# Performance work log

Hardware: AMD Instinct MI355X
Metric: run time of the kernel (lower is better)

Reference implementation:

```python
import jax, jax.numpy as jnp
import numpy as np

N, E, D_IN, D_H, D_OUT = 8000, 256000, 128, 128, 64
TEMP = 10.0       # config temperature.value (non-learnable)
WEIGHT = 1.0      # config weight.value (non-learnable)
LN_EPS = 1e-5


def _gcn_conv(x, W, b, src, dst, n):
    # PyG GCNConv: add self loops, sym-normalized aggregation, then bias.
    h = x @ W
    loop = jnp.arange(n)
    s = jnp.concatenate([src, loop])
    d = jnp.concatenate([dst, loop])
    deg = jnp.zeros((n,), h.dtype).at[d].add(1.0)
    dinv = jax.lax.rsqrt(jnp.maximum(deg, 1e-12))
    norm = dinv[s] * dinv[d]                       # [E+N]
    out = jax.ops.segment_sum(h[s] * norm[:, None], d, num_segments=n)
    return out + b


def _entropy_gradient(x, A, temperature, normalize):
    # E_i = 0.5 * sum_j A_ij ||x_i - x_j||^2  (dense adjacency, as in repo)
    sq = jnp.sum(x * x, axis=1)                    # [N]
    Ax = A @ x                                     # [N,d]
    deg = A.sum(axis=1)                            # [N]
    En = 0.5 * (deg * sq + A @ sq - 2.0 * jnp.sum(x * Ax, axis=1))
    if normalize:
        En = En / (jnp.max(En) + 1e-12)
    logits = -En / temperature
    P = jax.nn.softmax(logits)
    logP = jax.nn.log_softmax(logits)
    S = -jnp.sum(P * logP)
    c = P * (logP + S) / temperature               # dS/dE_k
    # dS/dx_i = c_i*(deg_i x_i - (Ax)_i) + (A^T c)_i x_i - (A^T (c*x))_i
    ATc = A.T @ c
    return (c[:, None] * (deg[:, None] * x - Ax)
            + ATc[:, None] * x - A.T @ (c[:, None] * x))


def _layer_norm(x, gamma, beta):
    mu = jnp.mean(x, axis=-1, keepdims=True)
    var = jnp.mean(jnp.square(x - mu), axis=-1, keepdims=True)
    return (x - mu) * jax.lax.rsqrt(var + LN_EPS) * gamma + beta


def setup_inputs() -> dict:
    key = jax.random.key(0)
    ks = jax.random.split(key, 6)
    def w(k, i, o):
        return jax.random.normal(k, (i, o), jnp.float32) / np.sqrt(i).astype(np.float32)
    return {
        "x": jax.random.normal(ks[0], (N, D_IN), jnp.float32),
        "edge_index": jax.random.randint(ks[1], (2, E), 0, N),
        "W1": w(ks[2], D_IN, D_H), "b1": jnp.zeros((D_H,), jnp.float32),
        "W2": w(ks[3], D_H, D_H), "b2": jnp.zeros((D_H,), jnp.float32),
        "W_out": w(ks[4], D_H, D_OUT), "b_out": jnp.zeros((D_OUT,), jnp.float32),
        "ln_gamma": jnp.ones((D_H,), jnp.float32),
        "ln_beta": jnp.zeros((D_H,), jnp.float32),
    }


def reference(x, edge_index, W1, b1, W2, b2, W_out, b_out, ln_gamma, ln_beta):
    n = x.shape[0]
    src, dst = edge_index[0], edge_index[1]
    # dense adjacency (to_dense_adj sums duplicate edges)
    A = jnp.zeros((n, n), x.dtype).at[src, dst].add(1.0)
    for W, b in ((W1, b1), (W2, b2)):
        h = _gcn_conv(x, W, b, src, dst, n)
        eg = jax.lax.stop_gradient(_entropy_gradient(h, A, TEMP, True))
        h = h + WEIGHT * eg
        h = jax.nn.relu(h)
        x = _layer_norm(h, ln_gamma, ln_beta)
    embedding = _gcn_conv(x, W_out, b_out, src, dst, n)
    return embedding
```

## Files before the change

kernel.cpp:

```cpp
#include <hip/hip_runtime.h>
#include <hip/hip_bf16.h>

#define DH 128

static constexpr float TEMP_ = 10.0f;
static constexpr float LN_EPS_ = 1e-5f;

__device__ __forceinline__ unsigned short f2bf(float f) {
  union { float f; unsigned int i; } v; v.f = f;
  unsigned int b = v.i + 0x7FFFu + ((v.i >> 16) & 1u);
  return (unsigned short)(b >> 16);
}
__device__ __forceinline__ void dec2(unsigned int u, float& lo, float& hi) {
  union { unsigned int i; float f; } a, b;
  a.i = u << 16; b.i = u & 0xFFFF0000u;
  lo = a.f; hi = b.f;
}
__device__ __forceinline__ void dec8(uint4 u, float* o) {
  dec2(u.x, o[0], o[1]); dec2(u.y, o[2], o[3]);
  dec2(u.z, o[4], o[5]); dec2(u.w, o[6], o[7]);
}
__device__ __forceinline__ unsigned int pack2(float lo, float hi) {
  return (unsigned int)f2bf(lo) | ((unsigned int)f2bf(hi) << 16);
}

__device__ __forceinline__ float grp_sum16(float v) {
  #pragma unroll
  for (int o = 8; o > 0; o >>= 1) v += __shfl_down(v, o, 16);
  return __shfl(v, 0, 16);
}

__device__ __forceinline__ float blkred(float v, float* s4) {
  const int t = threadIdx.x;
  #pragma unroll
  for (int o = 32; o > 0; o >>= 1) v += __shfl_down(v, o, 64);
  __syncthreads();
  if ((t & 63) == 0) s4[t >> 6] = v;
  __syncthreads();
  float r = (s4[0] + s4[1]) + (s4[2] + s4[3]);
  __syncthreads();
  return r;
}

__global__ void k_hist(const int* __restrict__ ei, int E, int* cnt_d, int* cnt_s) {
  for (int e = blockIdx.x * 256 + threadIdx.x; e < E; e += gridDim.x * 256) {
    atomicAdd(&cnt_s[ei[e]], 1);
    atomicAdd(&cnt_d[ei[E + e]], 1);
  }
}

__global__ __launch_bounds__(1024) void k_scan(int* cnt_d, int* cnt_s,
                                               int* off_d, int* off_s,
                                               float* dinv, float* dego, int n) {
  __shared__ int wsum[16];
  const int t = threadIdx.x;
  const int dir = blockIdx.x;
  int* cnt = dir ? cnt_s : cnt_d;
  int* off = dir ? off_s : off_d;
  const int PT = (n + 1023) >> 10;
  const int i0 = t * PT;
  int c[8];
  int tot = 0;
  #pragma unroll
  for (int j = 0; j < 8; ++j) {
    const int i = i0 + j;
    c[j] = (j < PT && i < n) ? cnt[i] : 0;
    tot += c[j];
  }
  const int lane = t & 63, w = t >> 6;
  int v = tot;
  #pragma unroll
  for (int o = 1; o < 64; o <<= 1) {
    int u = __shfl_up(v, o, 64);
    if (lane >= o) v += u;
  }
  if (lane == 63) wsum[w] = v;
  __syncthreads();
  int wbase = 0;
  #pragma unroll
  for (int k = 0; k < 16; ++k) wbase += (k < w) ? wsum[k] : 0;
  int excl = wbase + v - tot;
  #pragma unroll
  for (int j = 0; j < 8; ++j) {
    const int i = i0 + j;
    if (j < PT && i < n) {
      off[i] = excl;
      if (dir == 0) dinv[i] = rsqrtf((float)c[j] + 1.0f);
      else          dego[i] = (float)c[j];
      cnt[i] = 0;
      excl += c[j];
    }
  }
  if (t == 0) {
    int s = 0;
    #pragma unroll
    for (int k = 0; k < 16; ++k) s += wsum[k];
    off[n] = s;
  }
}

__global__ __launch_bounds__(256) void k_gemm1_fill(const float* __restrict__ X,
                                                    const float* __restrict__ W,
                                                    const float* __restrict__ dinv,
                                                    unsigned short* __restrict__ Hb,
                                                    const int* __restrict__ ei, int E,
                                                    const int* __restrict__ off_d,
                                                    const int* __restrict__ off_s,
                                                    int* cnt_d, int* cnt_s,
                                                    int* idx_d, int* idx_s, int NT) {
  __shared__ float Ws[64 * DH];
  __shared__ float xs[16 * 128];
  const int t = threadIdx.x;
  if ((int)blockIdx.x < NT) {
    const int row0 = blockIdx.x * 16;
    const float4* xg = (const float4*)(X + row0 * 128);
    float4* xs4 = (float4*)xs;
    xs4[t] = xg[t];
    xs4[t + 256] = xg[t + 256];
    const int c = t & 127, rg = t >> 7;
    float acc[8];
    #pragma unroll
    for (int r = 0; r < 8; ++r) acc[r] = 0.f;
    for (int kt = 0; kt < 2; ++kt) {
      __syncthreads();
      for (int i = t; i < 64 * DH; i += 256) Ws[i] = W[kt * 64 * DH + i];
      __syncthreads();
      for (int k = 0; k < 64; ++k) {
        float wv = Ws[k * DH + c];
        #pragma unroll
        for (int r = 0; r < 8; ++r)
          acc[r] += xs[(rg * 8 + r) * 128 + kt * 64 + k] * wv;
      }
    }
    #pragma unroll
    for (int r = 0; r < 8; ++r) {
      const int row = row0 + rg * 8 + r;
      Hb[row * DH + c] = f2bf(dinv[row] * acc[r]);
    }
  } else {
    const int nb = gridDim.x - NT;
    for (int e = (blockIdx.x - NT) * 256 + t; e < E; e += nb * 256) {
      int s = ei[e], d = ei[E + e];
      int p = atomicAdd(&cnt_d[d], 1);
      idx_d[off_d[d] + p] = s;
      int q = atomicAdd(&cnt_s[s], 1);
      idx_s[off_s[s] + q] = d;
    }
  }
}

__global__ __launch_bounds__(256) void k_conv_agg(const unsigned short* __restrict__ Hb,
                                                  const float* __restrict__ dinv,
                                                  const float* __restrict__ b,
                                                  const int* __restrict__ off_d,
                                                  const int* __restrict__ idx_d,
                                                  float* __restrict__ G,
                                                  unsigned short* __restrict__ Gb,
                                                  float* __restrict__ sq) {
  const int lane = threadIdx.x & 15;
  const int i = blockIdx.x * 16 + (threadIdx.x >> 4);
  const uint4* Hv = (const uint4*)Hb;
  const float di = dinv[i];
  float acc[8];
  dec8(Hv[i * 16 + lane], acc);
  int o = off_d[i];
  const int oe = off_d[i + 1];
  for (; o + 8 <= oe; o += 8) {
    int s[8]; uint4 r[8];
    #pragma unroll
    for (int j = 0; j < 8; ++j) s[j] = idx_d[o + j];
    #pragma unroll
    for (int j = 0; j < 8; ++j) r[j] = Hv[s[j] * 16 + lane];
    #pragma unroll
    for (int j = 0; j < 8; ++j) {
      float t8[8]; dec8(r[j], t8);
      #pragma unroll
      for (int k = 0; k < 8; ++k) acc[k] += t8[k];
    }
  }
  for (; o < oe; ++o) {
    int s = idx_d[o];
    float t8[8]; dec8(Hv[s * 16 + lane], t8);
    #pragma unroll
    for (int k = 0; k < 8; ++k) acc[k] += t8[k];
  }
  const float4 b0 = ((const float4*)b)[lane * 2];
  const float4 b1 = ((const float4*)b)[lane * 2 + 1];
  float gi[8];
  gi[0] = fmaf(di, acc[0], b0.x); gi[1] = fmaf(di, acc[1], b0.y);
  gi[2] = fmaf(di, acc[2], b0.z); gi[3] = fmaf(di, acc[3], b0.w);
  gi[4] = fmaf(di, acc[4], b1.x); gi[5] = fmaf(di, acc[5], b1.y);
  gi[6] = fmaf(di, acc[6], b1.z); gi[7] = fmaf(di, acc[7], b1.w);
  ((float4*)G)[i * 32 + lane * 2]     = make_float4(gi[0], gi[1], gi[2], gi[3]);
  ((float4*)G)[i * 32 + lane * 2 + 1] = make_float4(gi[4], gi[5], gi[6], gi[7]);
  uint4 gp;
  gp.x = pack2(gi[0], gi[1]); gp.y = pack2(gi[2], gi[3]);
  gp.z = pack2(gi[4], gi[5]); gp.w = pack2(gi[6], gi[7]);
  ((uint4*)Gb)[i * 16 + lane] = gp;
  float s2 = 0.f;
  #pragma unroll
  for (int k = 0; k < 8; ++k) s2 += gi[k] * gi[k];
  s2 = grp_sum16(s2);
  if (lane == 0) sq[i] = s2;
}

__global__ __launch_bounds__(256) void k_ax_en(const float* __restrict__ G,
                                               const unsigned short* __restrict__ Gb,
                                               const float* __restrict__ sq,
                                               const float* __restrict__ dego,
                                               const int* __restrict__ off_s,
                                               const int* __restrict__ idx_s,
                                               float* __restrict__ Ax,
                                               float* __restrict__ En,
                                               float* __restrict__ gmax) {
  __shared__ float smax[16];
  const int lane = threadIdx.x & 15;
  const int i = blockIdx.x * 16 + (threadIdx.x >> 4);
  const uint4* Gv = (const uint4*)Gb;
  float axf[8];
  #pragma unroll
  for (int k = 0; k < 8; ++k) axf[k] = 0.f;
  float asq = 0.f;
  int o = off_s[i];
  const int oe = off_s[i + 1];
  for (; o + 8 <= oe; o += 8) {
    int s[8]; float qv[8]; uint4 r[8];
    #pragma unroll
    for (int j = 0; j < 8; ++j) s[j] = idx_s[o + j];
    #pragma unroll
    for (int j = 0; j < 8; ++j) { r[j] = Gv[s[j] * 16 + lane]; qv[j] = sq[s[j]]; }
    #pragma unroll
    for (int j = 0; j < 8; ++j) {
      float t8[8]; dec8(r[j], t8);
      asq += qv[j];
      #pragma unroll
      for (int k = 0; k < 8; ++k) axf[k] += t8[k];
    }
  }
  for (; o < oe; ++o) {
    int s = idx_s[o];
    float t8[8]; dec8(Gv[s * 16 + lane], t8);
    asq += sq[s];
    #pragma unroll
    for (int k = 0; k < 8; ++k) axf[k] += t8[k];
  }
  ((float4*)Ax)[i * 32 + lane * 2]     = make_float4(axf[0], axf[1], axf[2], axf[3]);
  ((float4*)Ax)[i * 32 + lane * 2 + 1] = make_float4(axf[4], axf[5], axf[6], axf[7]);
  const float4 g0 = ((const float4*)G)[i * 32 + lane * 2];
  const float4 g1 = ((const float4*)G)[i * 32 + lane * 2 + 1];
  float dot = g0.x * axf[0] + g0.y * axf[1] + g0.z * axf[2] + g0.w * axf[3]
            + g1.x * axf[4] + g1.y * axf[5] + g1.z * axf[6] + g1.w * axf[7];
  dot = grp_sum16(dot);
  if (lane == 0) {
    float en = 0.5f * (dego[i] * sq[i] + asq - 2.f * dot);
    En[i] = en;
    smax[threadIdx.x >> 4] = en;
  }
  __syncthreads();
  if (threadIdx.x == 0) {
    float m = smax[0];
    #pragma unroll
    for (int k = 1; k < 16; ++k) m = fmaxf(m, smax[k]);
    atomicMax((int*)gmax, __float_as_int(m));
  }
}

template <int DOUT>
__global__ __launch_bounds__(256) void k_combine_gemm(const float* __restrict__ G,
                                                      const unsigned short* __restrict__ Gb,
                                                      const float* __restrict__ Ax,
                                                      const float* __restrict__ En,
                                                      const float* __restrict__ dego,
                                                      const float* __restrict__ dinv,
                                                      const int* __restrict__ off_d,
                                                      const int* __restrict__ idx_d,
                                                      const float* __restrict__ gamma,
                                                      const float* __restrict__ beta,
                                                      const float* __restrict__ W,
                                                      unsigned short* __restrict__ Hb,
                                                      const float* __restrict__ gmaxp,
                                                      int n) {
  __shared__ float Ws[64 * DOUT];
  __shared__ float xs[16 * 128];
  __shared__ float s4[4];
  const int t = threadIdx.x;
  const float m = gmaxp[0];
  const float invden = -1.0f / ((m + 1e-12f) * TEMP_);
  float se = 0.f, sl = 0.f;
  const float4* En4 = (const float4*)En;
  for (int k = t; k < (n >> 2); k += 256) {
    float4 e4 = En4[k];
    float l0 = e4.x * invden, l1 = e4.y * invden;
    float l2 = e4.z * invden, l3 = e4.w * invden;
    float e0 = __expf(l0), e1 = __expf(l1), e2 = __expf(l2), e3 = __expf(l3);
    se += (e0 + e1) + (e2 + e3);
    sl += (e0 * l0 + e1 * l1) + (e2 * l2 + e3 * l3);
  }
  se = blkred(se, s4);
  sl = blkred(sl, s4);
  const float logZ = __logf(se);
  const float S = logZ - sl / se;
  const float cmul = (1.0f / se) * (1.0f / TEMP_);
  const float cadd = S - logZ;

  const int lane = t & 15;
  const int i = blockIdx.x * 16 + (t >> 4);
  const uint4* Gv = (const uint4*)Gb;
  const float4 g0 = ((const float4*)G)[i * 32 + lane * 2];
  const float4 g1 = ((const float4*)G)[i * 32 + lane * 2 + 1];
  const float gi[8] = { g0.x, g0.y, g0.z, g0.w, g1.x, g1.y, g1.z, g1.w };
  float tf[8];
  #pragma unroll
  for (int k = 0; k < 8; ++k) tf[k] = 0.f;
  float atc = 0.f;
  int o = off_d[i];
  const int oe = off_d[i + 1];
  for (; o + 8 <= oe; o += 8) {
    int s[8]; float ev[8]; uint4 r[8];
    #pragma unroll
    for (int j = 0; j < 8; ++j) s[j] = idx_d[o + j];
    #pragma unroll
    for (int j = 0; j < 8; ++j) { r[j] = Gv[s[j] * 16 + lane]; ev[j] = En[s[j]]; }
    #pragma unroll
    for (int j = 0; j < 8; ++j) {
      float ls = ev[j] * invden;
      float cs = __expf(ls) * cmul * (ls + cadd);
      atc += cs;
      float t8[8]; dec8(r[j], t8);
      #pragma unroll
      for (int k = 0; k < 8; ++k) tf[k] = fmaf(cs, t8[k], tf[k]);
    }
  }
  for (; o < oe; ++o) {
    int s = idx_d[o];
    float ls = En[s] * invden;
    float cs = __expf(ls) * cmul * (ls + cadd);
    atc += cs;
    float t8[8]; dec8(Gv[s * 16 + lane], t8);
    #pragma unroll
    for (int k = 0; k < 8; ++k) tf[k] = fmaf(cs, t8[k], tf[k]);
  }
  const float li_i = En[i] * invden;
  const float ci = __expf(li_i) * cmul * (li_i + cadd);
  const float dg = dego[i];
  const float4 a0 = ((const float4*)Ax)[i * 32 + lane * 2];
  const float4 a1 = ((const float4*)Ax)[i * 32 + lane * 2 + 1];
  const float axi[8] = { a0.x, a0.y, a0.z, a0.w, a1.x, a1.y, a1.z, a1.w };
  float v[8];
  float ssum = 0.f;
  #pragma unroll
  for (int k = 0; k < 8; ++k) {
    v[k] = fmaxf(gi[k] + ci * (dg * gi[k] - axi[k]) + atc * gi[k] - tf[k], 0.f);
    ssum += v[k];
  }
  float mu = grp_sum16(ssum) * (1.f / 128.f);
  float vsum = 0.f;
  #pragma unroll
  for (int k = 0; k < 8; ++k) {
    v[k] -= mu;
    vsum += v[k] * v[k];
  }
  float var = grp_sum16(vsum) * (1.f / 128.f);
  float rs = rsqrtf(var + LN_EPS_);
  const float4 ga0 = ((const float4*)gamma)[lane * 2];
  const float4 ga1 = ((const float4*)gamma)[lane * 2 + 1];
  const float4 be0 = ((const float4*)beta)[lane * 2];
  const float4 be1 = ((const float4*)beta)[lane * 2 + 1];
  float4 o0, o1;
  o0.x = fmaf(v[0] * rs, ga0.x, be0.x); o0.y = fmaf(v[1] * rs, ga0.y, be0.y);
  o0.z = fmaf(v[2] * rs, ga0.z, be0.z); o0.w = fmaf(v[3] * rs, ga0.w, be0.w);
  o1.x = fmaf(v[4] * rs, ga1.x, be1.x); o1.y = fmaf(v[5] * rs, ga1.y, be1.y);
  o1.z = fmaf(v[6] * rs, ga1.z, be1.z); o1.w = fmaf(v[7] * rs, ga1.w, be1.w);

  float* xrow = xs + (t >> 4) * 128 + lane * 8;
  ((float4*)xrow)[0] = o0;
  ((float4*)xrow)[1] = o1;

  const int row0 = blockIdx.x * 16;
  constexpr int RPT = (16 * DOUT) / 256;
  const int c = t % DOUT;
  const int rg = t / DOUT;
  float acc[RPT];
  #pragma unroll
  for (int r = 0; r < RPT; ++r) acc[r] = 0.f;
  for (int kt = 0; kt < 2; ++kt) {
    if (kt) __syncthreads();
    for (int idx = t; idx < 64 * DOUT; idx += 256) Ws[idx] = W[kt * 64 * DOUT + idx];
    __syncthreads();
    for (int k = 0; k < 64; ++k) {
      float wv = Ws[k * DOUT + c];
      #pragma unroll
      for (int r = 0; r < RPT; ++r)
        acc[r] += xs[(rg * RPT + r) * 128 + kt * 64 + k] * wv;
    }
  }
  #pragma unroll
  for (int r = 0; r < RPT; ++r) {
    const int row = row0 + rg * RPT + r;
    Hb[row * DOUT + c] = f2bf(dinv[row] * acc[r]);
  }
}

__global__ __launch_bounds__(256) void k_final_agg(const unsigned short* __restrict__ Hb,
                                                   const float* __restrict__ dinv,
                                                   const float* __restrict__ bout,
                                                   const int* __restrict__ off_d,
                                                   const int* __restrict__ idx_d,
                                                   float* __restrict__ out) {
  const int lane = threadIdx.x & 7;
  const int i = blockIdx.x * 32 + (threadIdx.x >> 3);
  const uint4* Hv = (const uint4*)Hb;
  const float di = dinv[i];
  float acc[8];
  dec8(Hv[i * 8 + lane], acc);
  int o = off_d[i];
  const int oe = off_d[i + 1];
  for (; o + 8 <= oe; o += 8) {
    int s[8]; uint4 r[8];
    #pragma unroll
    for (int j = 0; j < 8; ++j) s[j] = idx_d[o + j];
    #pragma unroll
    for (int j = 0; j < 8; ++j) r[j] = Hv[s[j] * 8 + lane];
    #pragma unroll
    for (int j = 0; j < 8; ++j) {
      float t8[8]; dec8(r[j], t8);
      #pragma unroll
      for (int k = 0; k < 8; ++k) acc[k] += t8[k];
    }
  }
  for (; o < oe; ++o) {
    int s = idx_d[o];
    float t8[8]; dec8(Hv[s * 8 + lane], t8);
    #pragma unroll
    for (int k = 0; k < 8; ++k) acc[k] += t8[k];
  }
  const float4 b0 = ((const float4*)bout)[lane * 2];
  const float4 b1 = ((const float4*)bout)[lane * 2 + 1];
  float4 r0, r1;
  r0.x = fmaf(di, acc[0], b0.x); r0.y = fmaf(di, acc[1], b0.y);
  r0.z = fmaf(di, acc[2], b0.z); r0.w = fmaf(di, acc[3], b0.w);
  r1.x = fmaf(di, acc[4], b1.x); r1.y = fmaf(di, acc[5], b1.y);
  r1.z = fmaf(di, acc[6], b1.z); r1.w = fmaf(di, acc[7], b1.w);
  ((float4*)out)[i * 16 + lane * 2]     = r0;
  ((float4*)out)[i * 16 + lane * 2 + 1] = r1;
}

extern "C" void kernel_launch(void* const* d_in, const int* in_sizes, int n_in,
                              void* d_out, int out_size, void* d_ws, size_t ws_size,
                              hipStream_t stream) {
  const float* x    = (const float*)d_in[0];
  const int*   ei   = (const int*)d_in[1];
  const float* W1   = (const float*)d_in[2];
  const float* b1   = (const float*)d_in[3];
  const float* W2   = (const float*)d_in[4];
  const float* b2   = (const float*)d_in[5];
  const float* Wout = (const float*)d_in[6];
  const float* bout = (const float*)d_in[7];
  const float* gam  = (const float*)d_in[8];
  const float* bet  = (const float*)d_in[9];
  float* out = (float*)d_out;

  const int N = in_sizes[0] / DH;
  const int E = in_sizes[1] / 2;

  float* ws = (float*)d_ws;
  float* G  = ws;   ws += N * DH;
  float* Ax = ws;   ws += N * DH;
  float* sq = ws;   ws += N;
  float* En = ws;   ws += N;
  float* dinv = ws; ws += N;
  float* dego = ws; ws += N;
  unsigned short* Hb = (unsigned short*)ws; ws += N * DH / 2;
  unsigned short* Gb = (unsigned short*)ws; ws += N * DH / 2;
  int* cnt_d  = (int*)ws; ws += N;
  int* cnt_s  = (int*)ws; ws += N;
  float* gmax = (float*)ws; ws += 2;
  int* off_d  = (int*)ws; ws += N + 4;
  int* off_s  = (int*)ws; ws += N + 4;
  int* idx_d  = (int*)ws; ws += E;
  int* idx_s  = (int*)ws; ws += E;

  const int NT = N / 16;

  hipMemsetAsync(cnt_d, 0, (size_t)(2 * N + 2) * sizeof(int), stream);
  k_hist<<<256, 256, 0, stream>>>(ei, E, cnt_d, cnt_s);
  k_scan<<<2, 1024, 0, stream>>>(cnt_d, cnt_s, off_d, off_s, dinv, dego, N);
  k_gemm1_fill<<<NT + (E + 255) / 256, 256, 0, stream>>>(x, W1, dinv, Hb, ei, E,
                                                         off_d, off_s, cnt_d, cnt_s,
                                                         idx_d, idx_s, NT);

  k_conv_agg<<<N / 16, 256, 0, stream>>>(Hb, dinv, b1, off_d, idx_d, G, Gb, sq);
  k_ax_en<<<N / 16, 256, 0, stream>>>(G, Gb, sq, dego, off_s, idx_s, Ax, En, gmax);
  k_combine_gemm<128><<<N / 16, 256, 0, stream>>>(G, Gb, Ax, En, dego, dinv, off_d,
                                                  idx_d, gam, bet, W2, Hb, gmax, N);
  k_conv_agg<<<N / 16, 256, 0, stream>>>(Hb, dinv, b2, off_d, idx_d, G, Gb, sq);
  k_ax_en<<<N / 16, 256, 0, stream>>>(G, Gb, sq, dego, off_s, idx_s, Ax, En, gmax + 1);
  k_combine_gemm<64><<<N / 16, 256, 0, stream>>>(G, Gb, Ax, En, dego, dinv, off_d,
                                                 idx_d, gam, bet, Wout, Hb, gmax + 1, N);
  k_final_agg<<<N / 32, 256, 0, stream>>>(Hb, dinv, bout, off_d, idx_d, out);
}
```

Measured before the change: 244.7 us.

## Pad CSR neighbor lists to multiples of 16 with zero sentinel row

Each node's CSR segment is rounded up to a multiple of 16 and the extra slots point at a sentinel row N, whose features and sq are zero and whose En is huge so its entropy weight vanishes. The gather loops then run with no scalar tail, in chunks of 16 (8 in combine), and load the next chunk's indices while the current rows are being fetched. The last layer's projected features move to a separate buffer Hc. The cost is a new padding kernel, larger index arrays and wasted gathers on padded slots, which average about 7.5 per node against a mean degree of about 32.

```diff
diff --git a/kernel.cpp b/kernel.cpp
--- a/kernel.cpp
+++ b/kernel.cpp
@@ -59,13 +59,14 @@
   int* off = dir ? off_s : off_d;
   const int PT = (n + 1023) >> 10;
   const int i0 = t * PT;
-  int c[8];
+  int c[8], pc[8];
   int tot = 0;
   #pragma unroll
   for (int j = 0; j < 8; ++j) {
     const int i = i0 + j;
     c[j] = (j < PT && i < n) ? cnt[i] : 0;
-    tot += c[j];
+    pc[j] = (c[j] + 15) & ~15;
+    tot += pc[j];
   }
   const int lane = t & 63, w = t >> 6;
   int v = tot;
@@ -88,7 +89,7 @@
       if (dir == 0) dinv[i] = rsqrtf((float)c[j] + 1.0f);
       else          dego[i] = (float)c[j];
       cnt[i] = 0;
-      excl += c[j];
+      excl += pc[j];
     }
   }
   if (t == 0) {
@@ -149,6 +150,42 @@
   }
 }
 
+__global__ __launch_bounds__(256) void k_pad(const int* __restrict__ cnt_d,
+                                             const int* __restrict__ cnt_s,
+                                             const int* __restrict__ off_d,
+                                             const int* __restrict__ off_s,
+                                             int* idx_d, int* idx_s,
+                                             unsigned short* Hb, unsigned short* Gb,
+                                             unsigned short* Hc,
+                                             float* sq, float* En, int N) {
+  const int lane = threadIdx.x & 15;
+  const int u = blockIdx.x * 16 + (threadIdx.x >> 4);
+  if (u < N) {
+    const int o = off_d[u];
+    const int pd = off_d[u + 1] - o;
+    const int p = cnt_d[u] + lane;
+    if (p < pd) idx_d[o + p] = N;
+  } else if (u < 2 * N) {
+    const int i = u - N;
+    const int o = off_s[i];
+    const int pd = off_s[i + 1] - o;
+    const int p = cnt_s[i] + lane;
+    if (p < pd) idx_s[o + p] = N;
+  }
+  if (blockIdx.x == 0) {
+    const int t = threadIdx.x;
+    if (t < 64) {
+      ((unsigned int*)(Hb + (size_t)N * 128))[t] = 0u;
+      ((unsigned int*)(Gb + (size_t)N * 128))[t] = 0u;
+    } else if (t < 96) {
+      ((unsigned int*)(Hc + (size_t)N * 64))[t - 64] = 0u;
+    } else if (t == 96) {
+      sq[N] = 0.f;
+      En[N] = 3.0e38f;
+    }
+  }
+}
+
 __global__ __launch_bounds__(256) void k_conv_agg(const unsigned short* __restrict__ Hb,
                                                   const float* __restrict__ dinv,
                                                   const float* __restrict__ b,
@@ -165,24 +202,25 @@
   dec8(Hv[i * 16 + lane], acc);
   int o = off_d[i];
   const int oe = off_d[i + 1];
-  for (; o + 8 <= oe; o += 8) {
-    int s[8]; uint4 r[8];
-    #pragma unroll
-    for (int j = 0; j < 8; ++j) s[j] = idx_d[o + j];
-    #pragma unroll
-    for (int j = 0; j < 8; ++j) r[j] = Hv[s[j] * 16 + lane];
-    #pragma unroll
-    for (int j = 0; j < 8; ++j) {
+  int s[16];
+  if (o < oe) {
+    #pragma unroll
+    for (int j = 0; j < 16; ++j) s[j] = idx_d[o + j];
+  }
+  for (; o < oe; o += 16) {
+    uint4 r[16];
+    #pragma unroll
+    for (int j = 0; j < 16; ++j) r[j] = Hv[s[j] * 16 + lane];
+    if (o + 16 < oe) {
+      #pragma unroll
+      for (int j = 0; j < 16; ++j) s[j] = idx_d[o + 16 + j];
+    }
+    #pragma unroll
+    for (int j = 0; j < 16; ++j) {
       float t8[8]; dec8(r[j], t8);
       #pragma unroll
       for (int k = 0; k < 8; ++k) acc[k] += t8[k];
     }
-  }
-  for (; o < oe; ++o) {
-    int s = idx_d[o];
-    float t8[8]; dec8(Hv[s * 16 + lane], t8);
-    #pragma unroll
-    for (int k = 0; k < 8; ++k) acc[k] += t8[k];
   }
   const float4 b0 = ((const float4*)b)[lane * 2];
   const float4 b1 = ((const float4*)b)[lane * 2 + 1];
@@ -223,26 +261,28 @@
   float asq = 0.f;
   int o = off_s[i];
   const int oe = off_s[i + 1];
-  for (; o + 8 <= oe; o += 8) {
-    int s[8]; float qv[8]; uint4 r[8];
-    #pragma unroll
-    for (int j = 0; j < 8; ++j) s[j] = idx_s[o + j];
-    #pragma unroll
-    for (int j = 0; j < 8; ++j) { r[j] = Gv[s[j] * 16 + lane]; qv[j] = sq[s[j]]; }
-    #pragma unroll
-    for (int j = 0; j < 8; ++j) {
+  int s[16];
+  if (o < oe) {
+    #pragma unroll
+    for (int j = 0; j < 16; ++j) s[j] = idx_s[o + j];
+  }
+  for (; o < oe; o += 16) {
+    uint4 r[16]; float qv[16];
+    #pragma unroll
+    for (int j = 0; j < 16; ++j) r[j] = Gv[s[j] * 16 + lane];
+    #pragma unroll
+    for (int j = 0; j < 16; ++j) qv[j] = sq[s[j]];
+    if (o + 16 < oe) {
+      #pragma unroll
+      for (int j = 0; j < 16; ++j) s[j] = idx_s[o + 16 + j];
+    }
+    #pragma unroll
+    for (int j = 0; j < 16; ++j) {
       float t8[8]; dec8(r[j], t8);
       asq += qv[j];
       #pragma unroll
       for (int k = 0; k < 8; ++k) axf[k] += t8[k];
     }
-  }
-  for (; o < oe; ++o) {
-    int s = idx_s[o];
-    float t8[8]; dec8(Gv[s * 16 + lane], t8);
-    asq += sq[s];
-    #pragma unroll
-    for (int k = 0; k < 8; ++k) axf[k] += t8[k];
   }
   ((float4*)Ax)[i * 32 + lane * 2]     = make_float4(axf[0], axf[1], axf[2], axf[3]);
   ((float4*)Ax)[i * 32 + lane * 2 + 1] = make_float4(axf[4], axf[5], axf[6], axf[7]);
@@ -315,12 +355,21 @@
   float atc = 0.f;
   int o = off_d[i];
   const int oe = off_d[i + 1];
-  for (; o + 8 <= oe; o += 8) {
-    int s[8]; float ev[8]; uint4 r[8];
+  int s[8];
+  if (o < oe) {
     #pragma unroll
     for (int j = 0; j < 8; ++j) s[j] = idx_d[o + j];
-    #pragma unroll
-    for (int j = 0; j < 8; ++j) { r[j] = Gv[s[j] * 16 + lane]; ev[j] = En[s[j]]; }
+  }
+  for (; o < oe; o += 8) {
+    uint4 r[8]; float ev[8];
+    #pragma unroll
+    for (int j = 0; j < 8; ++j) r[j] = Gv[s[j] * 16 + lane];
+    #pragma unroll
+    for (int j = 0; j < 8; ++j) ev[j] = En[s[j]];
+    if (o + 8 < oe) {
+      #pragma unroll
+      for (int j = 0; j < 8; ++j) s[j] = idx_d[o + 8 + j];
+    }
     #pragma unroll
     for (int j = 0; j < 8; ++j) {
       float ls = ev[j] * invden;
@@ -330,15 +379,6 @@
       #pragma unroll
       for (int k = 0; k < 8; ++k) tf[k] = fmaf(cs, t8[k], tf[k]);
     }
-  }
-  for (; o < oe; ++o) {
-    int s = idx_d[o];
-    float ls = En[s] * invden;
-    float cs = __expf(ls) * cmul * (ls + cadd);
-    atc += cs;
-    float t8[8]; dec8(Gv[s * 16 + lane], t8);
-    #pragma unroll
-    for (int k = 0; k < 8; ++k) tf[k] = fmaf(cs, t8[k], tf[k]);
   }
   const float li_i = En[i] * invden;
   const float ci = __expf(li_i) * cmul * (li_i + cadd);
@@ -401,7 +441,7 @@
   }
 }
 
-__global__ __launch_bounds__(256) void k_final_agg(const unsigned short* __restrict__ Hb,
+__global__ __launch_bounds__(256) void k_final_agg(const unsigned short* __restrict__ Hc,
                                                    const float* __restrict__ dinv,
                                                    const float* __restrict__ bout,
                                                    const int* __restrict__ off_d,
@@ -409,30 +449,31 @@
                                                    float* __restrict__ out) {
   const int lane = threadIdx.x & 7;
   const int i = blockIdx.x * 32 + (threadIdx.x >> 3);
-  const uint4* Hv = (const uint4*)Hb;
+  const uint4* Hv = (const uint4*)Hc;
   const float di = dinv[i];
   float acc[8];
   dec8(Hv[i * 8 + lane], acc);
   int o = off_d[i];
   const int oe = off_d[i + 1];
-  for (; o + 8 <= oe; o += 8) {
-    int s[8]; uint4 r[8];
-    #pragma unroll
-    for (int j = 0; j < 8; ++j) s[j] = idx_d[o + j];
-    #pragma unroll
-    for (int j = 0; j < 8; ++j) r[j] = Hv[s[j] * 8 + lane];
-    #pragma unroll
-    for (int j = 0; j < 8; ++j) {
+  int s[16];
+  if (o < oe) {
+    #pragma unroll
+    for (int j = 0; j < 16; ++j) s[j] = idx_d[o + j];
+  }
+  for (; o < oe; o += 16) {
+    uint4 r[16];
+    #pragma unroll
+    for (int j = 0; j < 16; ++j) r[j] = Hv[s[j] * 8 + lane];
+    if (o + 16 < oe) {
+      #pragma unroll
+      for (int j = 0; j < 16; ++j) s[j] = idx_d[o + 16 + j];
+    }
+    #pragma unroll
+    for (int j = 0; j < 16; ++j) {
       float t8[8]; dec8(r[j], t8);
       #pragma unroll
       for (int k = 0; k < 8; ++k) acc[k] += t8[k];
     }
-  }
-  for (; o < oe; ++o) {
-    int s = idx_d[o];
-    float t8[8]; dec8(Hv[s * 8 + lane], t8);
-    #pragma unroll
-    for (int k = 0; k < 8; ++k) acc[k] += t8[k];
   }
   const float4 b0 = ((const float4*)bout)[lane * 2];
   const float4 b1 = ((const float4*)bout)[lane * 2 + 1];
@@ -462,32 +503,36 @@
 
   const int N = in_sizes[0] / DH;
   const int E = in_sizes[1] / 2;
+  const int EP = E + 16 * N;
 
   float* ws = (float*)d_ws;
   float* G  = ws;   ws += N * DH;
   float* Ax = ws;   ws += N * DH;
-  float* sq = ws;   ws += N;
-  float* En = ws;   ws += N;
+  float* sq = ws;   ws += N + 8;
+  float* En = ws;   ws += N + 8;
   float* dinv = ws; ws += N;
   float* dego = ws; ws += N;
-  unsigned short* Hb = (unsigned short*)ws; ws += N * DH / 2;
-  unsigned short* Gb = (unsigned short*)ws; ws += N * DH / 2;
+  unsigned short* Hb = (unsigned short*)ws; ws += (N + 1) * 64;
+  unsigned short* Gb = (unsigned short*)ws; ws += (N + 1) * 64;
+  unsigned short* Hc = (unsigned short*)ws; ws += (N + 1) * 32;
   int* cnt_d  = (int*)ws; ws += N;
   int* cnt_s  = (int*)ws; ws += N;
-  float* gmax = (float*)ws; ws += 2;
+  float* gmax = (float*)ws; ws += 8;
   int* off_d  = (int*)ws; ws += N + 4;
   int* off_s  = (int*)ws; ws += N + 4;
-  int* idx_d  = (int*)ws; ws += E;
-  int* idx_s  = (int*)ws; ws += E;
+  int* idx_d  = (int*)ws; ws += EP;
+  int* idx_s  = (int*)ws; ws += EP;
 
   const int NT = N / 16;
 
-  hipMemsetAsync(cnt_d, 0, (size_t)(2 * N + 2) * sizeof(int), stream);
+  hipMemsetAsync(cnt_d, 0, (size_t)(2 * N + 8) * sizeof(int), stream);
   k_hist<<<256, 256, 0, stream>>>(ei, E, cnt_d, cnt_s);
   k_scan<<<2, 1024, 0, stream>>>(cnt_d, cnt_s, off_d, off_s, dinv, dego, N);
   k_gemm1_fill<<<NT + (E + 255) / 256, 256, 0, stream>>>(x, W1, dinv, Hb, ei, E,
                                                          off_d, off_s, cnt_d, cnt_s,
                                                          idx_d, idx_s, NT);
+  k_pad<<<(2 * N + 15) / 16, 256, 0, stream>>>(cnt_d, cnt_s, off_d, off_s,
+                                               idx_d, idx_s, Hb, Gb, Hc, sq, En, N);
 
   k_conv_agg<<<N / 16, 256, 0, stream>>>(Hb, dinv, b1, off_d, idx_d, G, Gb, sq);
   k_ax_en<<<N / 16, 256, 0, stream>>>(G, Gb, sq, dego, off_s, idx_s, Ax, En, gmax);
@@ -496,6 +541,6 @@
   k_conv_agg<<<N / 16, 256, 0, stream>>>(Hb, dinv, b2, off_d, idx_d, G, Gb, sq);
   k_ax_en<<<N / 16, 256, 0, stream>>>(G, Gb, sq, dego, off_s, idx_s, Ax, En, gmax + 1);
   k_combine_gemm<64><<<N / 16, 256, 0, stream>>>(G, Gb, Ax, En, dego, dinv, off_d,
-                                                 idx_d, gam, bet, Wout, Hb, gmax + 1, N);
-  k_final_agg<<<N / 32, 256, 0, stream>>>(Hb, dinv, bout, off_d, idx_d, out);
-}
+                                                 idx_d, gam, bet, Wout, Hc, gmax + 1, N);
+  k_final_agg<<<N / 32, 256, 0, stream>>>(Hc, dinv, bout, off_d, idx_d, out);
+}
```

New measurement: 238.2 us. 2.7% less time.
